# Optimization experiments

Measured on AMD Instinct MI355X. Metric: run time of the kernel, lower is better.

Reference implementation:

```python
import jax, jax.numpy as jnp
import numpy as np

FILTER_WIDTH = 6


def setup_inputs() -> dict:
    key = jax.random.key(0)
    ks = jax.random.split(key, 9)
    V, E, H, C = 50000, 128, 128, 2
    B, S = 64, 512
    inputs = jax.random.randint(ks[0], (B, S), 0, V)
    lengths = jax.random.randint(ks[1], (B,), 1, S)
    embed_table = (jax.random.normal(ks[2], (V, E), jnp.float32) * 0.1).at[0].set(0.0)  # padding_idx=0
    s = 1.0 / np.sqrt(H)
    w_ih = jax.random.uniform(ks[3], (4 * H, E), jnp.float32, -s, s)
    w_hh = jax.random.uniform(ks[4], (4 * H, H), jnp.float32, -s, s)
    b_ih = jax.random.uniform(ks[5], (4 * H,), jnp.float32, -s, s)
    b_hh = jax.random.uniform(ks[6], (4 * H,), jnp.float32, -s, s)
    sf = 1.0 / np.sqrt(H)
    fc_w = jax.random.uniform(ks[7], (C, H), jnp.float32, -sf, sf)
    fc_b = jax.random.uniform(ks[8], (C,), jnp.float32, -sf, sf)
    return dict(inputs=inputs, lengths=lengths, embed_table=embed_table,
                w_ih=w_ih, w_hh=w_hh, b_ih=b_ih, b_hh=b_hh, fc_w=fc_w, fc_b=fc_b)


def reference(inputs, lengths, embed_table, w_ih, w_hh, b_ih, b_hh, fc_w, fc_b):
    # Dropouts are identity in eval mode (p set to 0).
    B, S = inputs.shape
    E = embed_table.shape[1]
    H = w_hh.shape[1]
    FW = FILTER_WIDTH
    W = S - FW + 1

    emb = embed_table[inputs]                                   # [B, S, E]
    idx = jnp.arange(W)[:, None] + jnp.arange(FW)[None, :]       # [W, FW]
    xw = emb[:, idx, :]                                          # [B, W, FW, E] sliding windows
    x = xw.reshape(B * W, FW, E).transpose(1, 0, 2)              # [FW, B*W, E] time-major

    bias = b_ih + b_hh

    def step(carry, xt):
        h, c = carry
        g = xt @ w_ih.T + h @ w_hh.T + bias                      # [B*W, 4H], gate order i,f,g,o
        i, f, gg, o = jnp.split(g, 4, axis=-1)
        c = jax.nn.sigmoid(f) * c + jax.nn.sigmoid(i) * jnp.tanh(gg)
        h = jax.nn.sigmoid(o) * jnp.tanh(c)
        return (h, c), None

    h0 = jnp.zeros((B * W, H), emb.dtype)
    (h_last, _), _ = jax.lax.scan(step, (h0, h0), x)             # final hidden per window
    feat = jnp.max(h_last.reshape(B, W, H), axis=1)              # max-pool over windows
    return feat @ fc_w.T + fc_b                                  # [B, num_class]
```

## Files before the change

kernel.cpp:

```cpp
#include <hip/hip_runtime.h>
#include <math.h>
#include <float.h>

#define Bn   64
#define Sn   512
#define FWn  6
#define Wn   507
#define WT   32
#define NTILE 16

#define PROWS   37
#define PSTRIDE 512

typedef __attribute__((ext_vector_type(8))) _Float16 half8;
typedef __attribute__((ext_vector_type(4))) _Float16 half4;
typedef __attribute__((ext_vector_type(4))) float f32x4;

__device__ __forceinline__ float sigf(float x)  {
    return __builtin_amdgcn_rcpf(1.0f + __expf(-x));
}
__device__ __forceinline__ float tanh_(float x) {
    return 1.0f - 2.0f * __builtin_amdgcn_rcpf(__expf(2.0f * x) + 1.0f);
}

__global__ void __launch_bounds__(256)
pack_w_kernel(const float* __restrict__ w_ih, const float* __restrict__ w_hh,
              _Float16* __restrict__ wih_p, _Float16* __restrict__ whh_p)
{
    const int idx = blockIdx.x * 256 + threadIdx.x;
    const int j  = idx & 7;
    const int L  = (idx >> 3) & 63;
    const int ks = (idx >> 9) & 3;
    const int nt = idx >> 11;
    const int row = nt * 16 + (L & 15);
    const int col = ks * 32 + (L >> 4) * 8 + j;
    wih_p[idx] = (_Float16)w_ih[row * 128 + col];
    whh_p[idx] = (_Float16)w_hh[row * 128 + col];
}

__global__ void __launch_bounds__(512, 4)
lstm_kernel(const int* __restrict__ inputs, const float* __restrict__ embed,
            const _Float16* __restrict__ wih_p, const _Float16* __restrict__ whh_p,
            const float* __restrict__ b_ih, const float* __restrict__ b_hh,
            float* __restrict__ partial)
{
    __shared__ __align__(16) _Float16 Pt[PROWS * PSTRIDE];
    __shared__ __align__(16) _Float16 hsA[2][2][2048];
    const int t    = threadIdx.x;
    const int L    = t & 63;
    const int ut   = t >> 6;
    const int b    = blockIdx.x >> 4;
    const int tile = blockIdx.x & 15;
    const int w0   = tile * WT;
    const int q  = L >> 4;
    const int ln = L & 15;
    const int j8 = L & 7;
    const int u  = ut * 16 + ln;

    {
        f32x4 accx[3][4];
#pragma unroll
        for (int g = 0; g < 4; ++g) {
            const float bg = b_ih[g * 128 + u] + b_hh[g * 128 + u];
            accx[0][g] = (f32x4){bg, bg, bg, bg};
            accx[1][g] = accx[0][g];
            accx[2][g] = accx[0][g];
        }
        int tok[3];
#pragma unroll
        for (int mt = 0; mt < 3; ++mt) {
            int s = w0 + mt * 16 + ln; s = s < 511 ? s : 511;
            tok[mt] = inputs[b * Sn + s];
        }
#pragma unroll
        for (int ks = 0; ks < 4; ++ks) {
            half8 ax[3];
#pragma unroll
            for (int mt = 0; mt < 3; ++mt) {
                const float* er = embed + (size_t)tok[mt] * 128 + ks * 32 + q * 8;
                float4 e0 = *(const float4*)er;
                float4 e1 = *(const float4*)(er + 4);
                half8 a;
                a[0] = (_Float16)e0.x; a[1] = (_Float16)e0.y;
                a[2] = (_Float16)e0.z; a[3] = (_Float16)e0.w;
                a[4] = (_Float16)e1.x; a[5] = (_Float16)e1.y;
                a[6] = (_Float16)e1.z; a[7] = (_Float16)e1.w;
                ax[mt] = a;
            }
#pragma unroll
            for (int g = 0; g < 4; ++g) {
                half8 bw = *(const half8*)(wih_p + ((size_t)((g * 8 + ut) * 4 + ks) * 64 + L) * 8);
#pragma unroll
                for (int mt = 0; mt < 3; ++mt)
                    accx[mt][g] = __builtin_amdgcn_mfma_f32_16x16x32_f16(ax[mt], bw, accx[mt][g], 0, 0, 0);
            }
        }
#pragma unroll
        for (int mt = 0; mt < 3; ++mt)
#pragma unroll
            for (int r = 0; r < 4; ++r) {
                const int sl = mt * 16 + q * 4 + r;
                if (sl < PROWS) {
                    half4 o;
                    o[0] = (_Float16)accx[mt][0][r];
                    o[1] = (_Float16)accx[mt][1][r];
                    o[2] = (_Float16)accx[mt][2][r];
                    o[3] = (_Float16)accx[mt][3][r];
                    *(half4*)&Pt[sl * PSTRIDE + u * 4] = o;
                }
            }
    }

    half8 whf[4][4];
#pragma unroll
    for (int g = 0; g < 4; ++g)
#pragma unroll
        for (int ks = 0; ks < 4; ++ks)
            whf[g][ks] = *(const half8*)(whh_p + ((size_t)((g * 8 + ut) * 4 + ks) * 64 + L) * 8);

    __syncthreads();

    const int ks_h = ut >> 1;
    const int qp   = (ut & 1) * 2 + (ln >> 3);

    float cst[2][4] = {{0.f, 0.f, 0.f, 0.f}, {0.f, 0.f, 0.f, 0.f}};
    float hh[2][4];

    for (int st = 0; st < FWn; ++st) {
        if (st > 0) __syncthreads();
#pragma unroll
        for (int sub = 0; sub < 2; ++sub) {
            f32x4 acc[4];
#pragma unroll
            for (int r = 0; r < 4; ++r) {
                half4 pv = *(const half4*)&Pt[(sub * 16 + q * 4 + r + st) * PSTRIDE + u * 4];
                acc[0][r] = (float)pv[0]; acc[1][r] = (float)pv[1];
                acc[2][r] = (float)pv[2]; acc[3][r] = (float)pv[3];
            }
            if (st > 0) {
                const _Float16* hb = hsA[(st + 1) & 1][sub];
#pragma unroll
                for (int ks = 0; ks < 4; ++ks) {
                    half8 ah = *(const half8*)(hb + (ks * 64 + L) * 8);
#pragma unroll
                    for (int g = 0; g < 4; ++g)
                        acc[g] = __builtin_amdgcn_mfma_f32_16x16x32_f16(ah, whf[g][ks], acc[g], 0, 0, 0);
                }
            }
            _Float16* buf = hsA[st & 1][sub];
#pragma unroll
            for (int r = 0; r < 4; ++r) {
                float ii = sigf(acc[0][r]);
                float ff = sigf(acc[1][r]);
                float gg = tanh_(acc[2][r]);
                float oo = sigf(acc[3][r]);
                float cc = ff * cst[sub][r] + ii * gg;
                cst[sub][r] = cc;
                hh[sub][r] = oo * tanh_(cc);
                if (st < FWn - 1)
                    buf[ks_h * 512 + (qp * 16 + q * 4 + r) * 8 + j8] = (_Float16)hh[sub][r];
            }
        }
    }

    float mv = -FLT_MAX;
#pragma unroll
    for (int sub = 0; sub < 2; ++sub)
#pragma unroll
        for (int r = 0; r < 4; ++r) {
            const int w = w0 + sub * 16 + q * 4 + r;
            if (w < Wn) mv = fmaxf(mv, hh[sub][r]);
        }
    mv = fmaxf(mv, __shfl_xor(mv, 16));
    mv = fmaxf(mv, __shfl_xor(mv, 32));
    if (q == 0)
        partial[(size_t)(b * NTILE + tile) * 128 + u] = mv;
}

__global__ void __launch_bounds__(128)
final_kernel(const float* __restrict__ partial, const float* __restrict__ fc_w,
             const float* __restrict__ fc_b, float* __restrict__ out)
{
    const int b = blockIdx.x;
    const int u = threadIdx.x;
    float m = -FLT_MAX;
#pragma unroll
    for (int tl = 0; tl < NTILE; ++tl)
        m = fmaxf(m, partial[(size_t)(b * NTILE + tl) * 128 + u]);
    float v0 = m * fc_w[u];
    float v1 = m * fc_w[128 + u];
#pragma unroll
    for (int off = 1; off < 64; off <<= 1) {
        v0 += __shfl_xor(v0, off);
        v1 += __shfl_xor(v1, off);
    }
    __shared__ float red[2][2];
    if ((u & 63) == 0) { red[u >> 6][0] = v0; red[u >> 6][1] = v1; }
    __syncthreads();
    if (u == 0) {
        out[b * 2 + 0] = red[0][0] + red[1][0] + fc_b[0];
        out[b * 2 + 1] = red[0][1] + red[1][1] + fc_b[1];
    }
}

extern "C" void kernel_launch(void* const* d_in, const int* in_sizes, int n_in,
                              void* d_out, int out_size, void* d_ws, size_t ws_size,
                              hipStream_t stream)
{
    const int*   inputs = (const int*)d_in[0];
    const float* embed  = (const float*)d_in[2];
    const float* w_ih   = (const float*)d_in[3];
    const float* w_hh   = (const float*)d_in[4];
    const float* b_ih   = (const float*)d_in[5];
    const float* b_hh   = (const float*)d_in[6];
    const float* fc_w   = (const float*)d_in[7];
    const float* fc_b   = (const float*)d_in[8];
    float* out = (float*)d_out;

    float*    partial = (float*)d_ws;
    _Float16* wih_p   = (_Float16*)(partial + Bn * NTILE * 128);
    _Float16* whh_p   = wih_p + 65536;

    pack_w_kernel<<<dim3(256), 256, 0, stream>>>(w_ih, w_hh, wih_p, whh_p);
    lstm_kernel<<<dim3(Bn * NTILE), 512, 0, stream>>>(inputs, embed, wih_p, whh_p,
                                                      b_ih, b_hh, partial);
    final_kernel<<<dim3(Bn), 128, 0, stream>>>(partial, fc_w, fc_b, out);
}
```

Baseline: 141.1 us.

## Keep input projections in registers with bpermute shifts; fold log2e into weights

The input-projection results now stay in packed fp16 registers instead of a 37-row LDS table. Each timestep's shifted window rows are fetched with ds_bpermute lane rotations, which removes the large shared buffer and one barrier. log2(e) scaling is folded into the packed weights and biases so the gate nonlinearities can use exp2 directly. The step loop is fully unrolled and the max-pool is fused into the last step. In exchange, register pressure rises and the row-selection logic becomes more complex.

```diff
diff --git a/kernel.cpp b/kernel.cpp
--- a/kernel.cpp
+++ b/kernel.cpp
@@ -9,18 +9,22 @@
 #define WT   32
 #define NTILE 16
 
-#define PROWS   37
-#define PSTRIDE 512
+#define LOG2E  1.4426950408889634f
+#define LOG2E2 2.8853900817779268f
 
 typedef __attribute__((ext_vector_type(8))) _Float16 half8;
 typedef __attribute__((ext_vector_type(4))) _Float16 half4;
+typedef __attribute__((ext_vector_type(2))) _Float16 half2t;
 typedef __attribute__((ext_vector_type(4))) float f32x4;
 
-__device__ __forceinline__ float sigf(float x)  {
-    return __builtin_amdgcn_rcpf(1.0f + __expf(-x));
-}
-__device__ __forceinline__ float tanh_(float x) {
-    return 1.0f - 2.0f * __builtin_amdgcn_rcpf(__expf(2.0f * x) + 1.0f);
+__device__ __forceinline__ float sigf(float y) {
+    return __builtin_amdgcn_rcpf(1.0f + __builtin_amdgcn_exp2f(-y));
+}
+__device__ __forceinline__ float tanhg(float y) {
+    return 1.0f - 2.0f * __builtin_amdgcn_rcpf(__builtin_amdgcn_exp2f(y) + 1.0f);
+}
+__device__ __forceinline__ float tanhc(float c) {
+    return 1.0f - 2.0f * __builtin_amdgcn_rcpf(__builtin_amdgcn_exp2f(c * LOG2E2) + 1.0f);
 }
 
 __global__ void __launch_bounds__(256)
@@ -34,8 +38,9 @@
     const int nt = idx >> 11;
     const int row = nt * 16 + (L & 15);
     const int col = ks * 32 + (L >> 4) * 8 + j;
-    wih_p[idx] = (_Float16)w_ih[row * 128 + col];
-    whh_p[idx] = (_Float16)w_hh[row * 128 + col];
+    const float sc = ((nt >> 3) == 2) ? LOG2E2 : LOG2E;
+    wih_p[idx] = (_Float16)(sc * w_ih[row * 128 + col]);
+    whh_p[idx] = (_Float16)(sc * w_hh[row * 128 + col]);
 }
 
 __global__ void __launch_bounds__(512, 4)
@@ -44,7 +49,6 @@
             const float* __restrict__ b_ih, const float* __restrict__ b_hh,
             float* __restrict__ partial)
 {
-    __shared__ __align__(16) _Float16 Pt[PROWS * PSTRIDE];
     __shared__ __align__(16) _Float16 hsA[2][2][2048];
     const int t    = threadIdx.x;
     const int L    = t & 63;
@@ -57,11 +61,14 @@
     const int j8 = L & 7;
     const int u  = ut * 16 + ln;
 
+    unsigned pxA[3][4], pxB[3][4];
+
     {
         f32x4 accx[3][4];
 #pragma unroll
         for (int g = 0; g < 4; ++g) {
-            const float bg = b_ih[g * 128 + u] + b_hh[g * 128 + u];
+            const float sc = (g == 2) ? LOG2E2 : LOG2E;
+            const float bg = sc * (b_ih[g * 128 + u] + b_hh[g * 128 + u]);
             accx[0][g] = (f32x4){bg, bg, bg, bg};
             accx[1][g] = accx[0][g];
             accx[2][g] = accx[0][g];
@@ -99,15 +106,10 @@
         for (int mt = 0; mt < 3; ++mt)
 #pragma unroll
             for (int r = 0; r < 4; ++r) {
-                const int sl = mt * 16 + q * 4 + r;
-                if (sl < PROWS) {
-                    half4 o;
-                    o[0] = (_Float16)accx[mt][0][r];
-                    o[1] = (_Float16)accx[mt][1][r];
-                    o[2] = (_Float16)accx[mt][2][r];
-                    o[3] = (_Float16)accx[mt][3][r];
-                    *(half4*)&Pt[sl * PSTRIDE + u * 4] = o;
-                }
+                pxA[mt][r] = __builtin_bit_cast(unsigned,
+                    (half2t){(_Float16)accx[mt][0][r], (_Float16)accx[mt][1][r]});
+                pxB[mt][r] = __builtin_bit_cast(unsigned,
+                    (half2t){(_Float16)accx[mt][2][r], (_Float16)accx[mt][3][r]});
             }
     }
 
@@ -118,14 +120,18 @@
         for (int ks = 0; ks < 4; ++ks)
             whf[g][ks] = *(const half8*)(whh_p + ((size_t)((g * 8 + ut) * 4 + ks) * 64 + L) * 8);
 
-    __syncthreads();
+    const int rot16 = ((L + 16) & 63) << 2;
+    const int rot32 = ((L + 32) & 63) << 2;
+    const bool q0   = (q == 0);
+    const bool qlt2 = (q < 2);
 
     const int ks_h = ut >> 1;
     const int qp   = (ut & 1) * 2 + (ln >> 3);
 
     float cst[2][4] = {{0.f, 0.f, 0.f, 0.f}, {0.f, 0.f, 0.f, 0.f}};
-    float hh[2][4];
-
+    float mv = -FLT_MAX;
+
+#pragma unroll
     for (int st = 0; st < FWn; ++st) {
         if (st > 0) __syncthreads();
 #pragma unroll
@@ -133,9 +139,25 @@
             f32x4 acc[4];
 #pragma unroll
             for (int r = 0; r < 4; ++r) {
-                half4 pv = *(const half4*)&Pt[(sub * 16 + q * 4 + r + st) * PSTRIDE + u * 4];
-                acc[0][r] = (float)pv[0]; acc[1][r] = (float)pv[1];
-                acc[2][r] = (float)pv[2]; acc[3][r] = (float)pv[3];
+                const int k = st + r;
+                unsigned lo, hi;
+                if (k <= 3) {
+                    lo = pxA[sub][k]; hi = pxB[sub][k];
+                } else if (k <= 7) {
+                    unsigned sa = q0 ? pxA[sub + 1][k - 4] : pxA[sub][k - 4];
+                    unsigned sb = q0 ? pxB[sub + 1][k - 4] : pxB[sub][k - 4];
+                    lo = (unsigned)__builtin_amdgcn_ds_bpermute(rot16, (int)sa);
+                    hi = (unsigned)__builtin_amdgcn_ds_bpermute(rot16, (int)sb);
+                } else {
+                    unsigned sa = qlt2 ? pxA[sub + 1][0] : pxA[sub][0];
+                    unsigned sb = qlt2 ? pxB[sub + 1][0] : pxB[sub][0];
+                    lo = (unsigned)__builtin_amdgcn_ds_bpermute(rot32, (int)sa);
+                    hi = (unsigned)__builtin_amdgcn_ds_bpermute(rot32, (int)sb);
+                }
+                half2t l2 = __builtin_bit_cast(half2t, lo);
+                half2t h2 = __builtin_bit_cast(half2t, hi);
+                acc[0][r] = (float)l2[0]; acc[1][r] = (float)l2[1];
+                acc[2][r] = (float)h2[0]; acc[3][r] = (float)h2[1];
             }
             if (st > 0) {
                 const _Float16* hb = hsA[(st + 1) & 1][sub];
@@ -152,25 +174,21 @@
             for (int r = 0; r < 4; ++r) {
                 float ii = sigf(acc[0][r]);
                 float ff = sigf(acc[1][r]);
-                float gg = tanh_(acc[2][r]);
+                float gg = tanhg(acc[2][r]);
                 float oo = sigf(acc[3][r]);
                 float cc = ff * cst[sub][r] + ii * gg;
                 cst[sub][r] = cc;
-                hh[sub][r] = oo * tanh_(cc);
-                if (st < FWn - 1)
-                    buf[ks_h * 512 + (qp * 16 + q * 4 + r) * 8 + j8] = (_Float16)hh[sub][r];
-            }
-        }
-    }
-
-    float mv = -FLT_MAX;
-#pragma unroll
-    for (int sub = 0; sub < 2; ++sub)
-#pragma unroll
-        for (int r = 0; r < 4; ++r) {
-            const int w = w0 + sub * 16 + q * 4 + r;
-            if (w < Wn) mv = fmaxf(mv, hh[sub][r]);
-        }
+                float hv = oo * tanhc(cc);
+                if (st < FWn - 1) {
+                    buf[ks_h * 512 + (qp * 16 + q * 4 + r) * 8 + j8] = (_Float16)hv;
+                } else {
+                    const int w = w0 + sub * 16 + q * 4 + r;
+                    mv = fmaxf(mv, (w < Wn) ? hv : -FLT_MAX);
+                }
+            }
+        }
+    }
+
     mv = fmaxf(mv, __shfl_xor(mv, 16));
     mv = fmaxf(mv, __shfl_xor(mv, 32));
     if (q == 0)
```

Measured after the change: 261.3 us. 1.85x slower.

## Halve window tile per block and fold log2e scaling into weights for exp2 gates

Applied to the files above, without the earlier changes.

Window tile shrinks from 32 to 16, so the grid doubles to 2048 blocks, each doing a single 16-row MFMA sub-tile per step with less shared memory. This lowers per-block serial latency and raises parallelism, at the cost of recomputing more overlapping projection rows (21 of 16 instead of 37 of 32). Weights and biases are pre-scaled by log2e (2·log2e for the g gate) so the gates use raw exp2. The sigmoid·tanh products are merged so each needs one reciprocal, cutting transcendental work in the recurrence.

```diff
diff --git a/kernel.cpp b/kernel.cpp
--- a/kernel.cpp
+++ b/kernel.cpp
@@ -6,22 +6,18 @@
 #define Sn   512
 #define FWn  6
 #define Wn   507
-#define WT   32
-#define NTILE 16
-
-#define PROWS   37
+#define WT   16
+#define NTILE 32
+
+#define PROWS   21
 #define PSTRIDE 512
+
+#define LOG2E  1.4426950408889634f
+#define LOG2E2 2.8853900817779268f
 
 typedef __attribute__((ext_vector_type(8))) _Float16 half8;
 typedef __attribute__((ext_vector_type(4))) _Float16 half4;
 typedef __attribute__((ext_vector_type(4))) float f32x4;
-
-__device__ __forceinline__ float sigf(float x)  {
-    return __builtin_amdgcn_rcpf(1.0f + __expf(-x));
-}
-__device__ __forceinline__ float tanh_(float x) {
-    return 1.0f - 2.0f * __builtin_amdgcn_rcpf(__expf(2.0f * x) + 1.0f);
-}
 
 __global__ void __launch_bounds__(256)
 pack_w_kernel(const float* __restrict__ w_ih, const float* __restrict__ w_hh,
@@ -34,8 +30,9 @@
     const int nt = idx >> 11;
     const int row = nt * 16 + (L & 15);
     const int col = ks * 32 + (L >> 4) * 8 + j;
-    wih_p[idx] = (_Float16)w_ih[row * 128 + col];
-    whh_p[idx] = (_Float16)w_hh[row * 128 + col];
+    const float sc = ((nt >> 3) == 2) ? LOG2E2 : LOG2E;
+    wih_p[idx] = (_Float16)(sc * w_ih[row * 128 + col]);
+    whh_p[idx] = (_Float16)(sc * w_hh[row * 128 + col]);
 }
 
 __global__ void __launch_bounds__(512, 4)
@@ -45,12 +42,12 @@
             float* __restrict__ partial)
 {
     __shared__ __align__(16) _Float16 Pt[PROWS * PSTRIDE];
-    __shared__ __align__(16) _Float16 hsA[2][2][2048];
+    __shared__ __align__(16) _Float16 hsA[2][2048];
     const int t    = threadIdx.x;
     const int L    = t & 63;
     const int ut   = t >> 6;
-    const int b    = blockIdx.x >> 4;
-    const int tile = blockIdx.x & 15;
+    const int b    = blockIdx.x >> 5;
+    const int tile = blockIdx.x & 31;
     const int w0   = tile * WT;
     const int q  = L >> 4;
     const int ln = L & 15;
@@ -58,25 +55,25 @@
     const int u  = ut * 16 + ln;
 
     {
-        f32x4 accx[3][4];
+        f32x4 accx[2][4];
 #pragma unroll
         for (int g = 0; g < 4; ++g) {
-            const float bg = b_ih[g * 128 + u] + b_hh[g * 128 + u];
+            const float sc = (g == 2) ? LOG2E2 : LOG2E;
+            const float bg = sc * (b_ih[g * 128 + u] + b_hh[g * 128 + u]);
             accx[0][g] = (f32x4){bg, bg, bg, bg};
             accx[1][g] = accx[0][g];
-            accx[2][g] = accx[0][g];
-        }
-        int tok[3];
-#pragma unroll
-        for (int mt = 0; mt < 3; ++mt) {
+        }
+        int tok[2];
+#pragma unroll
+        for (int mt = 0; mt < 2; ++mt) {
             int s = w0 + mt * 16 + ln; s = s < 511 ? s : 511;
             tok[mt] = inputs[b * Sn + s];
         }
 #pragma unroll
         for (int ks = 0; ks < 4; ++ks) {
-            half8 ax[3];
-#pragma unroll
-            for (int mt = 0; mt < 3; ++mt) {
+            half8 ax[2];
+#pragma unroll
+            for (int mt = 0; mt < 2; ++mt) {
                 const float* er = embed + (size_t)tok[mt] * 128 + ks * 32 + q * 8;
                 float4 e0 = *(const float4*)er;
                 float4 e1 = *(const float4*)(er + 4);
@@ -91,12 +88,12 @@
             for (int g = 0; g < 4; ++g) {
                 half8 bw = *(const half8*)(wih_p + ((size_t)((g * 8 + ut) * 4 + ks) * 64 + L) * 8);
 #pragma unroll
-                for (int mt = 0; mt < 3; ++mt)
+                for (int mt = 0; mt < 2; ++mt)
                     accx[mt][g] = __builtin_amdgcn_mfma_f32_16x16x32_f16(ax[mt], bw, accx[mt][g], 0, 0, 0);
             }
         }
 #pragma unroll
-        for (int mt = 0; mt < 3; ++mt)
+        for (int mt = 0; mt < 2; ++mt)
 #pragma unroll
             for (int r = 0; r < 4; ++r) {
                 const int sl = mt * 16 + q * 4 + r;
@@ -123,54 +120,50 @@
     const int ks_h = ut >> 1;
     const int qp   = (ut & 1) * 2 + (ln >> 3);
 
-    float cst[2][4] = {{0.f, 0.f, 0.f, 0.f}, {0.f, 0.f, 0.f, 0.f}};
-    float hh[2][4];
+    float cst[4] = {0.f, 0.f, 0.f, 0.f};
+    float mv = -FLT_MAX;
 
     for (int st = 0; st < FWn; ++st) {
         if (st > 0) __syncthreads();
-#pragma unroll
-        for (int sub = 0; sub < 2; ++sub) {
-            f32x4 acc[4];
-#pragma unroll
-            for (int r = 0; r < 4; ++r) {
-                half4 pv = *(const half4*)&Pt[(sub * 16 + q * 4 + r + st) * PSTRIDE + u * 4];
-                acc[0][r] = (float)pv[0]; acc[1][r] = (float)pv[1];
-                acc[2][r] = (float)pv[2]; acc[3][r] = (float)pv[3];
-            }
-            if (st > 0) {
-                const _Float16* hb = hsA[(st + 1) & 1][sub];
-#pragma unroll
-                for (int ks = 0; ks < 4; ++ks) {
-                    half8 ah = *(const half8*)(hb + (ks * 64 + L) * 8);
-#pragma unroll
-                    for (int g = 0; g < 4; ++g)
-                        acc[g] = __builtin_amdgcn_mfma_f32_16x16x32_f16(ah, whf[g][ks], acc[g], 0, 0, 0);
-                }
-            }
-            _Float16* buf = hsA[st & 1][sub];
-#pragma unroll
-            for (int r = 0; r < 4; ++r) {
-                float ii = sigf(acc[0][r]);
-                float ff = sigf(acc[1][r]);
-                float gg = tanh_(acc[2][r]);
-                float oo = sigf(acc[3][r]);
-                float cc = ff * cst[sub][r] + ii * gg;
-                cst[sub][r] = cc;
-                hh[sub][r] = oo * tanh_(cc);
-                if (st < FWn - 1)
-                    buf[ks_h * 512 + (qp * 16 + q * 4 + r) * 8 + j8] = (_Float16)hh[sub][r];
-            }
-        }
-    }
-
-    float mv = -FLT_MAX;
-#pragma unroll
-    for (int sub = 0; sub < 2; ++sub)
+        f32x4 acc[4];
 #pragma unroll
         for (int r = 0; r < 4; ++r) {
-            const int w = w0 + sub * 16 + q * 4 + r;
-            if (w < Wn) mv = fmaxf(mv, hh[sub][r]);
-        }
+            half4 pv = *(const half4*)&Pt[(q * 4 + r + st) * PSTRIDE + u * 4];
+            acc[0][r] = (float)pv[0]; acc[1][r] = (float)pv[1];
+            acc[2][r] = (float)pv[2]; acc[3][r] = (float)pv[3];
+        }
+        if (st > 0) {
+            const _Float16* hb = hsA[(st + 1) & 1];
+#pragma unroll
+            for (int ks = 0; ks < 4; ++ks) {
+                half8 ah = *(const half8*)(hb + (ks * 64 + L) * 8);
+#pragma unroll
+                for (int g = 0; g < 4; ++g)
+                    acc[g] = __builtin_amdgcn_mfma_f32_16x16x32_f16(ah, whf[g][ks], acc[g], 0, 0, 0);
+            }
+        }
+        _Float16* buf = hsA[st & 1];
+#pragma unroll
+        for (int r = 0; r < 4; ++r) {
+            float a  = __builtin_amdgcn_exp2f(-acc[0][r]);
+            float cf = __builtin_amdgcn_exp2f(-acc[1][r]);
+            float bb = __builtin_amdgcn_exp2f(-acc[2][r]);
+            float co = __builtin_amdgcn_exp2f(-acc[3][r]);
+            float ft  = __builtin_amdgcn_rcpf(1.0f + cf);
+            float itg = (1.0f - bb) * __builtin_amdgcn_rcpf((1.0f + a) * (1.0f + bb));
+            float cc  = fmaf(cst[r], ft, itg);
+            cst[r] = cc;
+            float d  = __builtin_amdgcn_exp2f(-LOG2E2 * cc);
+            float hv = (1.0f - d) * __builtin_amdgcn_rcpf((1.0f + co) * (1.0f + d));
+            if (st < FWn - 1) {
+                buf[ks_h * 512 + (qp * 16 + q * 4 + r) * 8 + j8] = (_Float16)hv;
+            } else {
+                const int w = w0 + q * 4 + r;
+                mv = fmaxf(mv, (w < Wn) ? hv : -FLT_MAX);
+            }
+        }
+    }
+
     mv = fmaxf(mv, __shfl_xor(mv, 16));
     mv = fmaxf(mv, __shfl_xor(mv, 32));
     if (q == 0)
```

After: 141.4 us. About the same (+0.2%).
